# Optimization experiments

Hardware: AMD Instinct MI355X
Metric: run time of the kernel (lower is better)

The kernel has to match this reference:

```python
import jax, jax.numpy as jnp
import numpy as np

H = 2048      # hidden_size
NH = 16       # num_heads
HD = H // NH  # head_dim
B, T = 2, 2048


def setup_inputs() -> dict:
    key = jax.random.key(0)
    ks = jax.random.split(key, 5)
    s = 1.0 / np.sqrt(H)
    return {
        "x": jax.random.normal(ks[0], (B, T, H), dtype=jnp.float32),
        "wq": jax.random.normal(ks[1], (H, H), dtype=jnp.float32) * s,
        "bq": jnp.zeros((H,), dtype=jnp.float32),
        "wk": jax.random.normal(ks[2], (H, H), dtype=jnp.float32) * s,
        "bk": jnp.zeros((H,), dtype=jnp.float32),
        "wv": jax.random.normal(ks[3], (H, H), dtype=jnp.float32) * s,
        "bv": jnp.zeros((H,), dtype=jnp.float32),
        "wo": jax.random.normal(ks[4], (H, H), dtype=jnp.float32) * s,
        "bo": jnp.zeros((H,), dtype=jnp.float32),
    }


def reference(x, wq, bq, wk, bk, wv, bv, wo, bo):
    Bx, Tx, C = x.shape
    # projections (torch Linear: x @ W.T + b)
    q = x @ wq.T + bq
    k = x @ wk.T + bk
    v = x @ wv.T + bv
    # [B, T, H] -> [B, NH, T, HD]
    q = q.reshape(Bx, Tx, NH, HD).transpose(0, 2, 1, 3)
    k = k.reshape(Bx, Tx, NH, HD).transpose(0, 2, 1, 3)
    v = v.reshape(Bx, Tx, NH, HD).transpose(0, 2, 1, 3)
    scale = 1.0 / np.sqrt(HD).astype(np.float32)
    scores = jnp.einsum('bhqd,bhkd->bhqk', q, k) * scale  # [B, NH, T, T]
    causal = jnp.tril(jnp.ones((Tx, Tx), dtype=bool))
    scores = jnp.where(causal[None, None], scores, -jnp.inf)
    attn = jax.nn.softmax(scores, axis=-1)
    out = jnp.einsum('bhqk,bhkd->bhqd', attn, v)  # [B, NH, T, HD]
    out = out.transpose(0, 2, 1, 3).reshape(Bx, Tx, C)
    return out @ wo.T + bo
```

## Files before the change

kernel.cpp:

```cpp
#include <hip/hip_runtime.h>
#include <stdint.h>

constexpr int H_  = 2048;
constexpr int NH_ = 16;
constexpr int HD_ = 128;
constexpr int B_  = 2;
constexpr int T_  = 2048;
constexpr int M_  = B_ * T_;

typedef unsigned short u16;
typedef __bf16 bf16x8 __attribute__((ext_vector_type(8)));
typedef float  f32x4  __attribute__((ext_vector_type(4)));

__device__ __forceinline__ u16 f2bf(float f) {
  uint32_t u = __builtin_bit_cast(uint32_t, f);
  u += 0x7fffu + ((u >> 16) & 1u);
  return (u16)(u >> 16);
}

__device__ __forceinline__ void gload_lds16(const void* g, void* lds) {
  auto gp = (const __attribute__((address_space(1))) uint32_t*)(uintptr_t)g;
  auto lp = (__attribute__((address_space(3))) uint32_t*)(uint32_t)(uintptr_t)lds;
  __builtin_amdgcn_global_load_lds(gp, lp, 16, 0, 0);
}

__device__ __forceinline__ f32x4 mfma16(bf16x8 a, bf16x8 b, f32x4 c) {
  return __builtin_amdgcn_mfma_f32_16x16x32_bf16(a, b, c, 0, 0, 0);
}

__global__ __launch_bounds__(256) void cvt_kernel(const float* __restrict__ s,
                                                  u16* __restrict__ d, int n4) {
  int i = blockIdx.x * 256 + threadIdx.x;
  if (i < n4) {
    float4 v = ((const float4*)s)[i];
    ushort4 o;
    o.x = f2bf(v.x); o.y = f2bf(v.y); o.z = f2bf(v.z); o.w = f2bf(v.w);
    ((ushort4*)d)[i] = o;
  }
}

template <int OUTF32>
__global__ __launch_bounds__(256) void gemm_bt(const u16* __restrict__ A,
                                               const u16* __restrict__ Bm,
                                               const float* __restrict__ bias,
                                               void* __restrict__ Cout,
                                               int M, int N, int K) {
  __shared__ u16 As[2][128 * 64];
  __shared__ u16 Bs[2][128 * 64];
  const int tid = threadIdx.x;
  const int wave = tid >> 6, lane = tid & 63, l15 = lane & 15, lhi = lane >> 4;
  const int tm = blockIdx.x % (M >> 7), tn = blockIdx.x / (M >> 7);
  const int m0 = tm << 7, n0 = tn << 7;
  const int wr = wave >> 1, wc = wave & 1;
  const int NT = K >> 6;

  f32x4 acc[4][4] = {};

  auto stage = [&](int kt, int buf) {
#pragma unroll
    for (int is = 0; is < 4; ++is) {
      int o  = is * 4096 + tid * 16;
      int row = o >> 7;
      int sw  = o ^ (((o >> 7) & 7) << 4);
      int c8  = (sw >> 4) & 7;
      gload_lds16(A + (size_t)(m0 + row) * K + kt * 64 + c8 * 8,
                  &As[buf][0] + (is * 2048 + wave * 512));
      gload_lds16(Bm + (size_t)(n0 + row) * K + kt * 64 + c8 * 8,
                  &Bs[buf][0] + (is * 2048 + wave * 512));
    }
  };

  stage(0, 0);
  __syncthreads();
  int cur = 0;
  for (int kt = 0; kt < NT; ++kt) {
    if (kt + 1 < NT) stage(kt + 1, cur ^ 1);
#pragma unroll
    for (int kk = 0; kk < 2; ++kk) {
      bf16x8 af[4], bfr[4];
#pragma unroll
      for (int mi = 0; mi < 4; ++mi) {
        int row = wr * 64 + mi * 16 + l15;
        int ob  = (row * 128 + kk * 64 + lhi * 16) ^ ((row & 7) << 4);
        af[mi] = *(const bf16x8*)((const char*)&As[cur][0] + ob);
      }
#pragma unroll
      for (int ni = 0; ni < 4; ++ni) {
        int row = wc * 64 + ni * 16 + l15;
        int ob  = (row * 128 + kk * 64 + lhi * 16) ^ ((row & 7) << 4);
        bfr[ni] = *(const bf16x8*)((const char*)&Bs[cur][0] + ob);
      }
#pragma unroll
      for (int mi = 0; mi < 4; ++mi)
#pragma unroll
        for (int ni = 0; ni < 4; ++ni)
          acc[mi][ni] = mfma16(af[mi], bfr[ni], acc[mi][ni]);
    }
    __syncthreads();
    cur ^= 1;
  }

  float bv[4];
#pragma unroll
  for (int ni = 0; ni < 4; ++ni) bv[ni] = bias[n0 + wc * 64 + ni * 16 + l15];
#pragma unroll
  for (int mi = 0; mi < 4; ++mi) {
#pragma unroll
    for (int ni = 0; ni < 4; ++ni) {
      int n = n0 + wc * 64 + ni * 16 + l15;
#pragma unroll
      for (int r = 0; r < 4; ++r) {
        int m = m0 + wr * 64 + mi * 16 + lhi * 4 + r;
        float v = acc[mi][ni][r] + bv[ni];
        if (OUTF32)
          ((float*)Cout)[(size_t)m * N + n] = v;
        else
          ((u16*)Cout)[(size_t)m * N + n] = f2bf(v);
      }
    }
  }
}

__global__ __launch_bounds__(256) void transpose_v(const u16* __restrict__ V,
                                                   u16* __restrict__ Vt) {
  __shared__ u16 tile[32][33];
  int bh = blockIdx.z, b = bh >> 4, h = bh & 15;
  int t0 = blockIdx.x * 32, d0 = blockIdx.y * 32;
  int x = threadIdx.x, y = threadIdx.y;
#pragma unroll
  for (int k = 0; k < 4; ++k) {
    int t = y + k * 8;
    tile[t][x] = V[(size_t)(b * T_ + t0 + t) * H_ + h * HD_ + d0 + x];
  }
  __syncthreads();
#pragma unroll
  for (int k = 0; k < 4; ++k) {
    int d = y + k * 8;
    Vt[((size_t)(bh * HD_ + d0 + d)) * T_ + t0 + x] = tile[x][d];
  }
}

__global__ __launch_bounds__(256) void attn_kernel(const u16* __restrict__ Q,
                                                   const u16* __restrict__ K,
                                                   const u16* __restrict__ Vt,
                                                   u16* __restrict__ ctx) {
  __shared__ u16 Ks[2][64 * 128];
  __shared__ u16 Vs[2][128 * 64];
  __shared__ u16 Ps[4][1024];

  const int tid = threadIdx.x, wave = tid >> 6, lane = tid & 63;
  const int l15 = lane & 15, lhi = lane >> 4;

  const int bid = blockIdx.x;
  const int xcd = bid & 7, idx = bid >> 3;
  const int bh = xcd * 4 + (idx & 3);
  const int qi = idx >> 2;
  const int b = bh >> 4, h = bh & 15;
  const int nQB = T_ / 64;
  const int qbs[2] = {qi, nQB - 1 - qi};

  const float C1  = 0.08838834764831845f * 1.4426950408889634f;
  const float THR = 11.5f;
  const float NI  = -__builtin_inff();

  auto stage = [&](int buf, int kv0) {
#pragma unroll
    for (int is = 0; is < 4; ++is) {
      {
        int o_ = is * 4096 + tid * 16;
        int row = o_ >> 8;
        int sw = o_ ^ (((o_ >> 8) & 7) << 4);
        int c8 = (sw >> 4) & 15;
        gload_lds16(K + (size_t)(b * T_ + kv0 + row) * H_ + h * HD_ + c8 * 8,
                    &Ks[buf][0] + (is * 2048 + wave * 512));
      }
      {
        int o_ = is * 4096 + tid * 16;
        int row = o_ >> 7;
        int sw = o_ ^ (((o_ >> 7) & 7) << 4);
        int t8 = (sw >> 4) & 7;
        gload_lds16(Vt + (size_t)(bh * HD_ + row) * T_ + kv0 + t8 * 8,
                    &Vs[buf][0] + (is * 2048 + wave * 512));
      }
    }
  };

  stage(0, 0);
  asm volatile("s_waitcnt vmcnt(0)" ::: "memory");
  __builtin_amdgcn_s_barrier();
  asm volatile("" ::: "memory");
  int cur = 0;

  for (int s = 0; s < 2; ++s) {
    const int qb = qbs[s];
    const int q0 = qb * 64 + wave * 16;
    const int qrow = q0 + l15;

    bf16x8 qf[4];
    const u16* qbase = Q + (size_t)(b * T_ + q0 + l15) * H_ + h * HD_ + lhi * 8;
#pragma unroll
    for (int kk = 0; kk < 4; ++kk) qf[kk] = *(const bf16x8*)(qbase + kk * 32);

    f32x4 o[8] = {};
    float m2 = NI, lr = 0.f;

    for (int kvb = 0; kvb <= qb; ++kvb) {
      const int kv0 = kvb * 64;
      const bool has_next = (kvb < qb) || (s == 0);
      if (has_next) {
        stage(cur ^ 1, (kvb < qb) ? kv0 + 64 : 0);
        asm volatile("s_waitcnt vmcnt(8)" ::: "memory");
      } else {
        asm volatile("s_waitcnt vmcnt(0)" ::: "memory");
      }
      __builtin_amdgcn_s_barrier();
      asm volatile("" ::: "memory");

      f32x4 sv[4];
      __builtin_amdgcn_s_setprio(1);
#pragma unroll
      for (int kt = 0; kt < 4; ++kt) {
        f32x4 sacc = {0.f, 0.f, 0.f, 0.f};
#pragma unroll
        for (int kk = 0; kk < 4; ++kk) {
          int row = kt * 16 + l15;
          int ob = (row * 256 + kk * 64 + lhi * 16) ^ ((row & 7) << 4);
          bf16x8 kf = *(const bf16x8*)((const char*)&Ks[cur][0] + ob);
          sacc = mfma16(kf, qf[kk], sacc);
        }
        sv[kt] = sacc;
      }
      __builtin_amdgcn_s_setprio(0);

      float pmax2 = NI;
      if (kvb == qb) {
#pragma unroll
        for (int kt = 0; kt < 4; ++kt)
#pragma unroll
          for (int r = 0; r < 4; ++r) {
            int key = kv0 + kt * 16 + lhi * 4 + r;
            float z = sv[kt][r] * C1;
            z = (key <= qrow) ? z : NI;
            sv[kt][r] = z;
            pmax2 = fmaxf(pmax2, z);
          }
      } else {
#pragma unroll
        for (int kt = 0; kt < 4; ++kt)
#pragma unroll
          for (int r = 0; r < 4; ++r) {
            float z = sv[kt][r] * C1;
            sv[kt][r] = z;
            pmax2 = fmaxf(pmax2, z);
          }
      }
      pmax2 = fmaxf(pmax2, __shfl_xor(pmax2, 16));
      pmax2 = fmaxf(pmax2, __shfl_xor(pmax2, 32));

      if (__any(pmax2 - m2 > THR)) {
        float mn = fmaxf(m2, pmax2);
        float al = exp2f(m2 - mn);
        m2 = mn;
        lr *= al;
        float alo[4];
#pragma unroll
        for (int r = 0; r < 4; ++r) alo[r] = __shfl(al, lhi * 4 + r);
#pragma unroll
        for (int dt = 0; dt < 8; ++dt)
#pragma unroll
          for (int r = 0; r < 4; ++r) o[dt][r] *= alo[r];
      }

      float rs = 0.f;
#pragma unroll
      for (int kt = 0; kt < 4; ++kt)
#pragma unroll
        for (int r = 0; r < 4; ++r) {
          float p = exp2f(sv[kt][r] - m2);
          sv[kt][r] = p;
          rs += p;
        }
      rs += __shfl_xor(rs, 16);
      rs += __shfl_xor(rs, 32);
      lr += rs;

#pragma unroll
      for (int kt = 0; kt < 4; ++kt) {
        int slot = kt * 2 + (lhi >> 1);
        ushort4 pk;
        pk.x = f2bf(sv[kt][0]);
        pk.y = f2bf(sv[kt][1]);
        pk.z = f2bf(sv[kt][2]);
        pk.w = f2bf(sv[kt][3]);
        *(ushort4*)&Ps[wave][slot * 128 + ((l15 * 8) ^ ((slot & 7) << 3)) +
                             (lhi & 1) * 4] = pk;
      }
      asm volatile("" ::: "memory");

      __builtin_amdgcn_s_setprio(1);
#pragma unroll
      for (int ks = 0; ks < 2; ++ks) {
        int slot = ks * 4 + lhi;
        bf16x8 pf = *(const bf16x8*)&Ps[wave][slot * 128 +
                                              ((l15 * 8) ^ ((slot & 7) << 3))];
#pragma unroll
        for (int dt = 0; dt < 8; ++dt) {
          int row = dt * 16 + l15;
          int ob = (row * 128 + ks * 64 + lhi * 16) ^ ((row & 7) << 4);
          bf16x8 vf = *(const bf16x8*)((const char*)&Vs[cur][0] + ob);
          o[dt] = mfma16(pf, vf, o[dt]);
        }
      }
      __builtin_amdgcn_s_setprio(0);

      __builtin_amdgcn_s_barrier();
      asm volatile("" ::: "memory");
      cur ^= 1;
    }

    float invo[4];
    {
      float inv = 1.0f / lr;
#pragma unroll
      for (int r = 0; r < 4; ++r) invo[r] = __shfl(inv, lhi * 4 + r);
    }
#pragma unroll
    for (int dt = 0; dt < 8; ++dt)
#pragma unroll
      for (int r = 0; r < 4; ++r) {
        float v = o[dt][r] * invo[r];
        ctx[(size_t)(b * T_ + q0 + lhi * 4 + r) * H_ + h * HD_ + dt * 16 +
            l15] = f2bf(v);
      }
  }
}

extern "C" void kernel_launch(void* const* d_in, const int* in_sizes, int n_in,
                              void* d_out, int out_size, void* d_ws,
                              size_t ws_size, hipStream_t stream) {
  const float* x  = (const float*)d_in[0];
  const float* wq = (const float*)d_in[1];
  const float* bq = (const float*)d_in[2];
  const float* wk = (const float*)d_in[3];
  const float* bk = (const float*)d_in[4];
  const float* wv = (const float*)d_in[5];
  const float* bv = (const float*)d_in[6];
  const float* wo = (const float*)d_in[7];
  const float* bo = (const float*)d_in[8];

  char* ws = (char*)d_ws;
  constexpr size_t SZ_X = (size_t)M_ * H_ * 2;
  constexpr size_t SZ_W = (size_t)H_ * H_ * 2;
  u16* xb  = (u16*)(ws);
  u16* wqb = (u16*)(ws + SZ_X);
  u16* wkb = (u16*)(ws + SZ_X + 1 * SZ_W);
  u16* wvb = (u16*)(ws + SZ_X + 2 * SZ_W);
  u16* wob = (u16*)(ws + SZ_X + 3 * SZ_W);
  u16* Qb  = (u16*)(ws + 1 * SZ_X + 4 * SZ_W);
  u16* Kb  = (u16*)(ws + 2 * SZ_X + 4 * SZ_W);
  u16* Vb  = (u16*)(ws + 3 * SZ_X + 4 * SZ_W);
  u16* Vtb = (u16*)(ws + 4 * SZ_X + 4 * SZ_W);
  u16* ctx = xb;

  cvt_kernel<<<(M_ * H_) / 1024, 256, 0, stream>>>(x, xb, (M_ * H_) / 4);
  cvt_kernel<<<(H_ * H_) / 1024, 256, 0, stream>>>(wq, wqb, (H_ * H_) / 4);
  cvt_kernel<<<(H_ * H_) / 1024, 256, 0, stream>>>(wk, wkb, (H_ * H_) / 4);
  cvt_kernel<<<(H_ * H_) / 1024, 256, 0, stream>>>(wv, wvb, (H_ * H_) / 4);
  cvt_kernel<<<(H_ * H_) / 1024, 256, 0, stream>>>(wo, wob, (H_ * H_) / 4);

  gemm_bt<0><<<512, 256, 0, stream>>>(xb, wqb, bq, Qb, M_, H_, H_);
  gemm_bt<0><<<512, 256, 0, stream>>>(xb, wkb, bk, Kb, M_, H_, H_);
  gemm_bt<0><<<512, 256, 0, stream>>>(xb, wvb, bv, Vb, M_, H_, H_);

  transpose_v<<<dim3(T_ / 32, HD_ / 32, B_ * NH_), dim3(32, 8), 0, stream>>>(
      Vb, Vtb);

  attn_kernel<<<512, 256, 0, stream>>>(Qb, Kb, Vtb, ctx);

  gemm_bt<1><<<512, 256, 0, stream>>>(ctx, wob, bo, d_out, M_, H_, H_);
}
```

Measured before the change: 256.9 us.

## Fuse conversions, write V transposed from GEMM, relax K-loop barrier waits

After: 243.4 us. 1.06x faster.

```diff
diff --git a/kernel.cpp b/kernel.cpp
--- a/kernel.cpp
+++ b/kernel.cpp
@@ -28,18 +28,29 @@
   return __builtin_amdgcn_mfma_f32_16x16x32_bf16(a, b, c, 0, 0, 0);
 }
 
-__global__ __launch_bounds__(256) void cvt_kernel(const float* __restrict__ s,
-                                                  u16* __restrict__ d, int n4) {
-  int i = blockIdx.x * 256 + threadIdx.x;
-  if (i < n4) {
-    float4 v = ((const float4*)s)[i];
-    ushort4 o;
-    o.x = f2bf(v.x); o.y = f2bf(v.y); o.z = f2bf(v.z); o.w = f2bf(v.w);
-    ((ushort4*)d)[i] = o;
+__global__ __launch_bounds__(512) void cvt5_kernel(
+    const float4* __restrict__ x,  const float4* __restrict__ wq,
+    const float4* __restrict__ wk, const float4* __restrict__ wv,
+    const float4* __restrict__ wo, ushort4* __restrict__ dst) {
+  const int bid = blockIdx.x, tid = threadIdx.x;
+  const float4* src;
+  size_t idx, dof;
+  if (bid < 4096) {
+    src = x; idx = (size_t)bid * 512 + tid; dof = 0;
+  } else {
+    int w = (bid - 4096) >> 11;
+    int r = (bid - 4096) & 2047;
+    idx = (size_t)r * 512 + tid;
+    dof = 2097152u + (size_t)w * 1048576u;
+    src = (w == 0) ? wq : (w == 1) ? wk : (w == 2) ? wv : wo;
   }
-}
-
-template <int OUTF32>
+  float4 v = src[idx];
+  ushort4 o;
+  o.x = f2bf(v.x); o.y = f2bf(v.y); o.z = f2bf(v.z); o.w = f2bf(v.w);
+  dst[dof + idx] = o;
+}
+
+template <int OUTMODE>
 __global__ __launch_bounds__(256) void gemm_bt(const u16* __restrict__ A,
                                                const u16* __restrict__ Bm,
                                                const float* __restrict__ bias,
@@ -71,10 +82,16 @@
   };
 
   stage(0, 0);
-  __syncthreads();
   int cur = 0;
   for (int kt = 0; kt < NT; ++kt) {
-    if (kt + 1 < NT) stage(kt + 1, cur ^ 1);
+    if (kt + 1 < NT) {
+      stage(kt + 1, cur ^ 1);
+      asm volatile("s_waitcnt vmcnt(8)" ::: "memory");
+    } else {
+      asm volatile("s_waitcnt vmcnt(0)" ::: "memory");
+    }
+    __builtin_amdgcn_s_barrier();
+    asm volatile("" ::: "memory");
 #pragma unroll
     for (int kk = 0; kk < 2; ++kk) {
       bf16x8 af[4], bfr[4];
@@ -96,47 +113,49 @@
         for (int ni = 0; ni < 4; ++ni)
           acc[mi][ni] = mfma16(af[mi], bfr[ni], acc[mi][ni]);
     }
-    __syncthreads();
+    __builtin_amdgcn_s_barrier();
+    asm volatile("" ::: "memory");
     cur ^= 1;
   }
 
   float bv[4];
 #pragma unroll
   for (int ni = 0; ni < 4; ++ni) bv[ni] = bias[n0 + wc * 64 + ni * 16 + l15];
-#pragma unroll
-  for (int mi = 0; mi < 4; ++mi) {
-#pragma unroll
-    for (int ni = 0; ni < 4; ++ni) {
-      int n = n0 + wc * 64 + ni * 16 + l15;
-#pragma unroll
-      for (int r = 0; r < 4; ++r) {
-        int m = m0 + wr * 64 + mi * 16 + lhi * 4 + r;
-        float v = acc[mi][ni][r] + bv[ni];
-        if (OUTF32)
-          ((float*)Cout)[(size_t)m * N + n] = v;
-        else
-          ((u16*)Cout)[(size_t)m * N + n] = f2bf(v);
-      }
-    }
-  }
-}
-
-__global__ __launch_bounds__(256) void transpose_v(const u16* __restrict__ V,
-                                                   u16* __restrict__ Vt) {
-  __shared__ u16 tile[32][33];
-  int bh = blockIdx.z, b = bh >> 4, h = bh & 15;
-  int t0 = blockIdx.x * 32, d0 = blockIdx.y * 32;
-  int x = threadIdx.x, y = threadIdx.y;
-#pragma unroll
-  for (int k = 0; k < 4; ++k) {
-    int t = y + k * 8;
-    tile[t][x] = V[(size_t)(b * T_ + t0 + t) * H_ + h * HD_ + d0 + x];
-  }
-  __syncthreads();
-#pragma unroll
-  for (int k = 0; k < 4; ++k) {
-    int d = y + k * 8;
-    Vt[((size_t)(bh * HD_ + d0 + d)) * T_ + t0 + x] = tile[x][d];
+
+  if constexpr (OUTMODE == 2) {
+    const int b = m0 >> 11;
+    const int tbase = (m0 & 2047) + wr * 64 + lhi * 4;
+#pragma unroll
+    for (int mi = 0; mi < 4; ++mi) {
+#pragma unroll
+      for (int ni = 0; ni < 4; ++ni) {
+        int n = n0 + wc * 64 + ni * 16 + l15;
+        ushort4 pk;
+        pk.x = f2bf(acc[mi][ni][0] + bv[ni]);
+        pk.y = f2bf(acc[mi][ni][1] + bv[ni]);
+        pk.z = f2bf(acc[mi][ni][2] + bv[ni]);
+        pk.w = f2bf(acc[mi][ni][3] + bv[ni]);
+        *(ushort4*)((u16*)Cout + (size_t)(b * 2048 + n) * T_ + tbase +
+                    mi * 16) = pk;
+      }
+    }
+  } else {
+#pragma unroll
+    for (int mi = 0; mi < 4; ++mi) {
+#pragma unroll
+      for (int ni = 0; ni < 4; ++ni) {
+        int n = n0 + wc * 64 + ni * 16 + l15;
+#pragma unroll
+        for (int r = 0; r < 4; ++r) {
+          int m = m0 + wr * 64 + mi * 16 + lhi * 4 + r;
+          float v = acc[mi][ni][r] + bv[ni];
+          if (OUTMODE == 1)
+            ((float*)Cout)[(size_t)m * N + n] = v;
+          else
+            ((u16*)Cout)[(size_t)m * N + n] = f2bf(v);
+        }
+      }
+    }
   }
 }
 
@@ -358,22 +377,16 @@
   u16* wob = (u16*)(ws + SZ_X + 3 * SZ_W);
   u16* Qb  = (u16*)(ws + 1 * SZ_X + 4 * SZ_W);
   u16* Kb  = (u16*)(ws + 2 * SZ_X + 4 * SZ_W);
-  u16* Vb  = (u16*)(ws + 3 * SZ_X + 4 * SZ_W);
-  u16* Vtb = (u16*)(ws + 4 * SZ_X + 4 * SZ_W);
+  u16* Vtb = (u16*)(ws + 3 * SZ_X + 4 * SZ_W);
   u16* ctx = xb;
 
-  cvt_kernel<<<(M_ * H_) / 1024, 256, 0, stream>>>(x, xb, (M_ * H_) / 4);
-  cvt_kernel<<<(H_ * H_) / 1024, 256, 0, stream>>>(wq, wqb, (H_ * H_) / 4);
-  cvt_kernel<<<(H_ * H_) / 1024, 256, 0, stream>>>(wk, wkb, (H_ * H_) / 4);
-  cvt_kernel<<<(H_ * H_) / 1024, 256, 0, stream>>>(wv, wvb, (H_ * H_) / 4);
-  cvt_kernel<<<(H_ * H_) / 1024, 256, 0, stream>>>(wo, wob, (H_ * H_) / 4);
+  cvt5_kernel<<<12288, 512, 0, stream>>>((const float4*)x, (const float4*)wq,
+                                         (const float4*)wk, (const float4*)wv,
+                                         (const float4*)wo, (ushort4*)ws);
 
   gemm_bt<0><<<512, 256, 0, stream>>>(xb, wqb, bq, Qb, M_, H_, H_);
   gemm_bt<0><<<512, 256, 0, stream>>>(xb, wkb, bk, Kb, M_, H_, H_);
-  gemm_bt<0><<<512, 256, 0, stream>>>(xb, wvb, bv, Vb, M_, H_, H_);
-
-  transpose_v<<<dim3(T_ / 32, HD_ / 32, B_ * NH_), dim3(32, 8), 0, stream>>>(
-      Vb, Vtb);
+  gemm_bt<2><<<512, 256, 0, stream>>>(xb, wvb, bv, Vtb, M_, H_, H_);
 
   attn_kernel<<<512, 256, 0, stream>>>(Qb, Kb, Vtb, ctx);
 
```
